# Kernel optimization log

Measured on AMD Instinct MI355X. Metric: run time of the kernel, lower is better.

The kernel has to match this reference:

```python
import jax, jax.numpy as jnp
import numpy as np

EPS = 1e-05
QN, QP = -128.0, 127.0


def setup_inputs() -> dict:
    key = jax.random.key(0)
    kx, kw = jax.random.split(key)
    x = jax.random.normal(kx, (4, 2048, 4096), dtype=jnp.float32)
    weight = jax.random.normal(kw, (4096, 4096), dtype=jnp.float32)  # [out, in]
    return {"x": x, "weight": weight}


def reference(x, weight):
    # --- per-token int8 activation quantization (activation_quant) ---
    # s: [B, S, 1], scale so that max(|x|) maps to 127
    s = QP / jnp.clip(jnp.max(jnp.abs(x), axis=-1, keepdims=True), 1e-05, None)
    q = jnp.clip(jnp.round(x * s), QN, QP)  # int8-valued, kept in float
    xq = q / s  # dequantized activations fed to the matmul

    # --- ternary weight quantization (terniarize + pack/unpack round-trip) ---
    scale_w = 1.0 / jnp.clip(jnp.mean(jnp.abs(weight)), EPS, None)
    tw = jnp.clip(jnp.round(weight * scale_w), -1.0, 1.0)  # ternary {-1,0,1}, [out, in]

    # --- bitmat: (xq) @ tw^T, then dequant by weight scale ---
    out = jnp.einsum('bsi,oi->bso', xq, tw) / scale_w
    return out
```

## Files before the change

### kernel.cpp

```cpp
#include <hip/hip_runtime.h>
#include <stdint.h>

#define K_DIM 4096
#define M_TOK 8192
#define N_OUT 4096

typedef int v4i __attribute__((ext_vector_type(4)));
typedef int v16i __attribute__((ext_vector_type(16)));


#define BAR()                                     \
    do {                                          \
        asm volatile("" ::: "memory");            \
        __builtin_amdgcn_s_barrier();             \
        asm volatile("" ::: "memory");            \
    } while (0)

__device__ __forceinline__ void gload_lds16(const void* g, void* l) {
    auto gp = reinterpret_cast<const __attribute__((address_space(1))) uint32_t*>(
        reinterpret_cast<uintptr_t>(g));
    auto lp = reinterpret_cast<__attribute__((address_space(3))) uint32_t*>(
        reinterpret_cast<uintptr_t>(l));
    __builtin_amdgcn_global_load_lds(gp, lp, 16, 0, 0);
}

__global__ __launch_bounds__(256) void quant_act(const float* __restrict__ x,
                                                 int8_t* __restrict__ q,
                                                 float* __restrict__ rs) {
    const int token = blockIdx.x;
    const int t = threadIdx.x;
    const float4* x4 = (const float4*)(x + (size_t)token * K_DIM);
    float4 v[4];
    float m = 0.0f;
#pragma unroll
    for (int r = 0; r < 4; ++r) {
        v[r] = x4[t + 256 * r];
        m = fmaxf(m, fmaxf(fmaxf(fabsf(v[r].x), fabsf(v[r].y)),
                           fmaxf(fabsf(v[r].z), fabsf(v[r].w))));
    }
#pragma unroll
    for (int off = 32; off; off >>= 1) m = fmaxf(m, __shfl_down(m, off, 64));
    __shared__ float wmax[4];
    __shared__ float smax;
    if ((t & 63) == 0) wmax[t >> 6] = m;
    __syncthreads();
    if (t == 0) smax = fmaxf(fmaxf(wmax[0], wmax[1]), fmaxf(wmax[2], wmax[3]));
    __syncthreads();
    const float s = 127.0f / fmaxf(smax, 1e-5f);
    char4* q4 = (char4*)(q + (size_t)token * K_DIM);
#pragma unroll
    for (int r = 0; r < 4; ++r) {
        float4 f = v[r];
        char4 c;
        c.x = (signed char)fminf(fmaxf(rintf(f.x * s), -128.0f), 127.0f);
        c.y = (signed char)fminf(fmaxf(rintf(f.y * s), -128.0f), 127.0f);
        c.z = (signed char)fminf(fmaxf(rintf(f.z * s), -128.0f), 127.0f);
        c.w = (signed char)fminf(fmaxf(rintf(f.w * s), -128.0f), 127.0f);
        q4[t + 256 * r] = c;
    }
    if (t == 0) rs[token] = 1.0f / s;
}

__global__ __launch_bounds__(256) void wabs_sum(const float* __restrict__ w,
                                                double* __restrict__ partial) {
    const size_t n4 = (size_t)N_OUT * K_DIM / 4;
    const size_t stride = (size_t)gridDim.x * 256;
    const float4* w4 = (const float4*)w;
    float sum = 0.0f;
    for (size_t j = (size_t)blockIdx.x * 256 + threadIdx.x; j < n4; j += stride) {
        float4 f = w4[j];
        sum += fabsf(f.x) + fabsf(f.y) + fabsf(f.z) + fabsf(f.w);
    }
    double d = (double)sum;
#pragma unroll
    for (int off = 32; off; off >>= 1) d += __shfl_down(d, off, 64);
    __shared__ double wsum[4];
    const int t = threadIdx.x;
    if ((t & 63) == 0) wsum[t >> 6] = d;
    __syncthreads();
    if (t == 0) partial[blockIdx.x] = wsum[0] + wsum[1] + wsum[2] + wsum[3];
}

__global__ __launch_bounds__(256) void ternarize(const float* __restrict__ w,
                                                 int8_t* __restrict__ tw,
                                                 const double* __restrict__ partial,
                                                 float* __restrict__ meanp) {
    const int t = threadIdx.x;
    double d = partial[t] + partial[t + 256] + partial[t + 512] + partial[t + 768];
#pragma unroll
    for (int off = 32; off; off >>= 1) d += __shfl_down(d, off, 64);
    __shared__ double pr[4];
    if ((t & 63) == 0) pr[t >> 6] = d;
    __syncthreads();
    const double tot = pr[0] + pr[1] + pr[2] + pr[3];
    const float mean = fmaxf((float)(tot * (1.0 / ((double)N_OUT * (double)K_DIM))), 1e-5f);
    const float sw = 1.0f / mean;
    if (blockIdx.x == 0 && t == 0) *meanp = mean;
    const float4* w4 = (const float4*)w;
    char4* t4 = (char4*)tw;
    const size_t base = (size_t)blockIdx.x * 1024 + t;
#pragma unroll
    for (int r = 0; r < 4; ++r) {
        float4 f = w4[base + r * 256];
        char4 c;
        c.x = (signed char)fminf(fmaxf(rintf(f.x * sw), -1.0f), 1.0f);
        c.y = (signed char)fminf(fmaxf(rintf(f.y * sw), -1.0f), 1.0f);
        c.z = (signed char)fminf(fmaxf(rintf(f.z * sw), -1.0f), 1.0f);
        c.w = (signed char)fminf(fmaxf(rintf(f.w * sw), -1.0f), 1.0f);
        t4[base + r * 256] = c;
    }
}

__global__ __launch_bounds__(512, 2) void gemm_i8(const int8_t* __restrict__ A,
                                                  const int8_t* __restrict__ B,
                                                  const float* __restrict__ rs,
                                                  const float* __restrict__ meanp,
                                                  float* __restrict__ out) {
    const int nwgx = N_OUT / 256;
    const int orig = blockIdx.y * nwgx + blockIdx.x;
    const int wg = (orig & 7) * 64 + (orig >> 3);
    const int bm = (wg / nwgx) * 256;
    const int bn = (wg % nwgx) * 256;

    __shared__ int8_t smem[4][2][16384];

    const int t0 = threadIdx.x;
    const int lane = t0 & 63;
    const int wave = t0 >> 6;
    const int wm = (wave >> 1) * 64;
    const int wn = (wave & 1) * 128;

    v16i accv[2][4] = {};

    const int R0 = t0 >> 2;
    const int scol = (((t0 & 3) ^ (R0 & 3) ^ ((R0 >> 2) & 3)) << 4);
    const int8_t* Ag = A + (size_t)(bm + R0) * K_DIM + scol;
    const int8_t* Bg = B + (size_t)(bn + R0) * K_DIM + scol;
    int8_t* ldst = &smem[0][0][0] + (size_t)t0 * 16;

    const int l31 = lane & 31;
    const int lh = lane >> 5;
    const int sx = (l31 & 3) ^ ((l31 >> 2) & 3);
    const int co0 = ((lh ^ sx) << 4);
    const int co1 = (((2 + lh) ^ sx) << 4);
    const int offA0 = (wm + l31) * 64;
    const int offA1 = (wm + 32 + l31) * 64;
    const int offB0 = (wn + l31) * 64;
    const int offB1 = (wn + 32 + l31) * 64;
    const int offB2 = (wn + 64 + l31) * 64;
    const int offB3 = (wn + 96 + l31) * 64;

#pragma unroll
    for (int pt = 0; pt < 3; ++pt) {
        const int k0 = pt * 64;
        int8_t* sb = ldst + pt * 32768;
        gload_lds16(Ag + k0, sb);
        gload_lds16(Ag + k0 + (size_t)128 * K_DIM, sb + 8192);
        gload_lds16(Bg + k0, sb + 16384);
        gload_lds16(Bg + k0 + (size_t)128 * K_DIM, sb + 24576);
    }
    asm volatile("s_waitcnt vmcnt(8)" ::: "memory");
    BAR();

    v4i ca0, ca1, cb0, cb1, cb2, cb3;
    {
        const int8_t* aB = &smem[0][0][0];
        const int8_t* bB = &smem[0][1][0];
        ca0 = *(const v4i*)(aB + offA0 + co0);
        ca1 = *(const v4i*)(aB + offA1 + co0);
        cb0 = *(const v4i*)(bB + offB0 + co0);
        cb1 = *(const v4i*)(bB + offB1 + co0);
        cb2 = *(const v4i*)(bB + offB2 + co0);
        cb3 = *(const v4i*)(bB + offB3 + co0);
    }

#pragma unroll 1
    for (int t = 0; t < 64; ++t) {
        const int slot = t & 3;
        const int8_t* aB = &smem[slot][0][0];
        const int8_t* bB = &smem[slot][1][0];

        if (t < 61) {
            const int ksg = (t + 3) * 64;
            int8_t* sb = ldst + ((t + 3) & 3) * 32768;
            gload_lds16(Ag + ksg, sb);
            gload_lds16(Ag + ksg + (size_t)128 * K_DIM, sb + 8192);
            gload_lds16(Bg + ksg, sb + 16384);
            gload_lds16(Bg + ksg + (size_t)128 * K_DIM, sb + 24576);
        }

        v4i na0 = *(const v4i*)(aB + offA0 + co1);
        v4i na1 = *(const v4i*)(aB + offA1 + co1);
        v4i nb0 = *(const v4i*)(bB + offB0 + co1);
        v4i nb1 = *(const v4i*)(bB + offB1 + co1);
        v4i nb2 = *(const v4i*)(bB + offB2 + co1);
        v4i nb3 = *(const v4i*)(bB + offB3 + co1);

        __builtin_amdgcn_s_setprio(1);
        accv[0][0] = __builtin_amdgcn_mfma_i32_32x32x32_i8(ca0, cb0, accv[0][0], 0, 0, 0);
        accv[1][0] = __builtin_amdgcn_mfma_i32_32x32x32_i8(ca1, cb0, accv[1][0], 0, 0, 0);
        accv[0][1] = __builtin_amdgcn_mfma_i32_32x32x32_i8(ca0, cb1, accv[0][1], 0, 0, 0);
        accv[1][1] = __builtin_amdgcn_mfma_i32_32x32x32_i8(ca1, cb1, accv[1][1], 0, 0, 0);
        accv[0][2] = __builtin_amdgcn_mfma_i32_32x32x32_i8(ca0, cb2, accv[0][2], 0, 0, 0);
        accv[1][2] = __builtin_amdgcn_mfma_i32_32x32x32_i8(ca1, cb2, accv[1][2], 0, 0, 0);
        accv[0][3] = __builtin_amdgcn_mfma_i32_32x32x32_i8(ca0, cb3, accv[0][3], 0, 0, 0);
        accv[1][3] = __builtin_amdgcn_mfma_i32_32x32x32_i8(ca1, cb3, accv[1][3], 0, 0, 0);
        __builtin_amdgcn_s_setprio(0);

        if (t < 61) asm volatile("s_waitcnt vmcnt(8)" ::: "memory");
        else if (t == 61) asm volatile("s_waitcnt vmcnt(4)" ::: "memory");
        else if (t == 62) asm volatile("s_waitcnt vmcnt(0)" ::: "memory");
        if (t < 63) {
            BAR();
            const int nslot = (t + 1) & 3;
            const int8_t* aN = &smem[nslot][0][0];
            const int8_t* bN = &smem[nslot][1][0];
            ca0 = *(const v4i*)(aN + offA0 + co0);
            ca1 = *(const v4i*)(aN + offA1 + co0);
            cb0 = *(const v4i*)(bN + offB0 + co0);
            cb1 = *(const v4i*)(bN + offB1 + co0);
            cb2 = *(const v4i*)(bN + offB2 + co0);
            cb3 = *(const v4i*)(bN + offB3 + co0);
        }

        __builtin_amdgcn_s_setprio(1);
        accv[0][0] = __builtin_amdgcn_mfma_i32_32x32x32_i8(na0, nb0, accv[0][0], 0, 0, 0);
        accv[1][0] = __builtin_amdgcn_mfma_i32_32x32x32_i8(na1, nb0, accv[1][0], 0, 0, 0);
        accv[0][1] = __builtin_amdgcn_mfma_i32_32x32x32_i8(na0, nb1, accv[0][1], 0, 0, 0);
        accv[1][1] = __builtin_amdgcn_mfma_i32_32x32x32_i8(na1, nb1, accv[1][1], 0, 0, 0);
        accv[0][2] = __builtin_amdgcn_mfma_i32_32x32x32_i8(na0, nb2, accv[0][2], 0, 0, 0);
        accv[1][2] = __builtin_amdgcn_mfma_i32_32x32x32_i8(na1, nb2, accv[1][2], 0, 0, 0);
        accv[0][3] = __builtin_amdgcn_mfma_i32_32x32x32_i8(na0, nb3, accv[0][3], 0, 0, 0);
        accv[1][3] = __builtin_amdgcn_mfma_i32_32x32x32_i8(na1, nb3, accv[1][3], 0, 0, 0);
        __builtin_amdgcn_s_setprio(0);
    }

    const float wmean = *meanp;
#pragma unroll
    for (int m = 0; m < 2; ++m) {
#pragma unroll
        for (int r = 0; r < 16; ++r) {
            const int row = bm + wm + m * 32 + (r & 3) + 8 * (r >> 2) + 4 * lh;
            const float scale = rs[row] * wmean;
            float* orow = out + (size_t)row * N_OUT + bn + wn + l31;
#pragma unroll
            for (int n = 0; n < 4; ++n)
                orow[n * 32] = (float)accv[m][n][r] * scale;
        }
    }
}

extern "C" void kernel_launch(void* const* d_in, const int* in_sizes, int n_in,
                              void* d_out, int out_size, void* d_ws, size_t ws_size,
                              hipStream_t stream) {
    const float* x = (const float*)d_in[0];
    const float* w = (const float*)d_in[1];
    float* out = (float*)d_out;
    char* ws = (char*)d_ws;
    int8_t* q = (int8_t*)ws;
    int8_t* tw = (int8_t*)(ws + 33554432);
    float* rs = (float*)(ws + 50331648);
    double* partial = (double*)(ws + 50364416);
    float* meanp = (float*)(ws + 50372608);

    hipLaunchKernelGGL(quant_act, dim3(M_TOK), dim3(256), 0, stream, x, q, rs);
    hipLaunchKernelGGL(wabs_sum, dim3(1024), dim3(256), 0, stream, w, partial);
    hipLaunchKernelGGL(ternarize, dim3((N_OUT * (size_t)K_DIM / 16) / 256), dim3(256), 0, stream, w, tw, partial, meanp);
    hipLaunchKernelGGL(gemm_i8, dim3(N_OUT / 256, M_TOK / 256), dim3(512), 0, stream, q, tw, rs, meanp, out);
}
```

Before: 405.1 us.

## Enlarge per-wave GEMM tile to 128x128 with four waves; one wave per token in quant

The GEMM now runs four waves per 256x256 workgroup instead of eight. Each wave computes a 128x128 sub-tile with 16 accumulators, which raises MFMA work per LDS fragment load and halves barrier participants. The cost is much higher register pressure (256 accumulator registers) and lower occupancy. The activation quant kernel now maps one wave per token and reduces with shuffle-xor only, which removes the shared memory and syncthreads step.

```diff
diff --git a/kernel.cpp b/kernel.cpp
--- a/kernel.cpp
+++ b/kernel.cpp
@@ -27,38 +27,32 @@
 __global__ __launch_bounds__(256) void quant_act(const float* __restrict__ x,
                                                  int8_t* __restrict__ q,
                                                  float* __restrict__ rs) {
-    const int token = blockIdx.x;
-    const int t = threadIdx.x;
+    const int token = blockIdx.x * 4 + (threadIdx.x >> 6);
+    const int lane = threadIdx.x & 63;
     const float4* x4 = (const float4*)(x + (size_t)token * K_DIM);
-    float4 v[4];
+    float4 v[16];
     float m = 0.0f;
 #pragma unroll
-    for (int r = 0; r < 4; ++r) {
-        v[r] = x4[t + 256 * r];
+    for (int r = 0; r < 16; ++r) {
+        v[r] = x4[lane + 64 * r];
         m = fmaxf(m, fmaxf(fmaxf(fabsf(v[r].x), fabsf(v[r].y)),
                            fmaxf(fabsf(v[r].z), fabsf(v[r].w))));
     }
 #pragma unroll
-    for (int off = 32; off; off >>= 1) m = fmaxf(m, __shfl_down(m, off, 64));
-    __shared__ float wmax[4];
-    __shared__ float smax;
-    if ((t & 63) == 0) wmax[t >> 6] = m;
-    __syncthreads();
-    if (t == 0) smax = fmaxf(fmaxf(wmax[0], wmax[1]), fmaxf(wmax[2], wmax[3]));
-    __syncthreads();
-    const float s = 127.0f / fmaxf(smax, 1e-5f);
+    for (int off = 32; off; off >>= 1) m = fmaxf(m, __shfl_xor(m, off, 64));
+    const float s = 127.0f / fmaxf(m, 1e-5f);
     char4* q4 = (char4*)(q + (size_t)token * K_DIM);
 #pragma unroll
-    for (int r = 0; r < 4; ++r) {
+    for (int r = 0; r < 16; ++r) {
         float4 f = v[r];
         char4 c;
         c.x = (signed char)fminf(fmaxf(rintf(f.x * s), -128.0f), 127.0f);
         c.y = (signed char)fminf(fmaxf(rintf(f.y * s), -128.0f), 127.0f);
         c.z = (signed char)fminf(fmaxf(rintf(f.z * s), -128.0f), 127.0f);
         c.w = (signed char)fminf(fmaxf(rintf(f.w * s), -128.0f), 127.0f);
-        q4[t + 256 * r] = c;
-    }
-    if (t == 0) rs[token] = 1.0f / s;
+        q4[lane + 64 * r] = c;
+    }
+    if (lane == 0) rs[token] = 1.0f / s;
 }
 
 __global__ __launch_bounds__(256) void wabs_sum(const float* __restrict__ w,
@@ -111,7 +105,7 @@
     }
 }
 
-__global__ __launch_bounds__(512, 2) void gemm_i8(const int8_t* __restrict__ A,
+__global__ __launch_bounds__(256, 1) void gemm_i8(const int8_t* __restrict__ A,
                                                   const int8_t* __restrict__ B,
                                                   const float* __restrict__ rs,
                                                   const float* __restrict__ meanp,
@@ -127,10 +121,10 @@
     const int t0 = threadIdx.x;
     const int lane = t0 & 63;
     const int wave = t0 >> 6;
-    const int wm = (wave >> 1) * 64;
+    const int wm = (wave >> 1) * 128;
     const int wn = (wave & 1) * 128;
 
-    v16i accv[2][4] = {};
+    v16i accv[4][4] = {};
 
     const int R0 = t0 >> 2;
     const int scol = (((t0 & 3) ^ (R0 & 3) ^ ((R0 >> 2) & 3)) << 4);
@@ -143,35 +137,37 @@
     const int sx = (l31 & 3) ^ ((l31 >> 2) & 3);
     const int co0 = ((lh ^ sx) << 4);
     const int co1 = (((2 + lh) ^ sx) << 4);
-    const int offA0 = (wm + l31) * 64;
-    const int offA1 = (wm + 32 + l31) * 64;
-    const int offB0 = (wn + l31) * 64;
-    const int offB1 = (wn + 32 + l31) * 64;
-    const int offB2 = (wn + 64 + l31) * 64;
-    const int offB3 = (wn + 96 + l31) * 64;
-
-#pragma unroll
-    for (int pt = 0; pt < 3; ++pt) {
-        const int k0 = pt * 64;
-        int8_t* sb = ldst + pt * 32768;
-        gload_lds16(Ag + k0, sb);
-        gload_lds16(Ag + k0 + (size_t)128 * K_DIM, sb + 8192);
-        gload_lds16(Bg + k0, sb + 16384);
-        gload_lds16(Bg + k0 + (size_t)128 * K_DIM, sb + 24576);
-    }
-    asm volatile("s_waitcnt vmcnt(8)" ::: "memory");
+    int offA[4], offB[4];
+#pragma unroll
+    for (int i = 0; i < 4; ++i) {
+        offA[i] = (wm + i * 32 + l31) * 64;
+        offB[i] = (wn + i * 32 + l31) * 64;
+    }
+
+#define STAGE(tile, sb)                                                       \
+    do {                                                                      \
+        const int k0_ = (tile) * 64;                                          \
+        _Pragma("unroll")                                                     \
+        for (int r_ = 0; r_ < 4; ++r_) {                                      \
+            gload_lds16(Ag + k0_ + (size_t)(64 * r_) * K_DIM, (sb) + r_ * 4096);          \
+            gload_lds16(Bg + k0_ + (size_t)(64 * r_) * K_DIM, (sb) + 16384 + r_ * 4096);  \
+        }                                                                     \
+    } while (0)
+
+#pragma unroll
+    for (int pt = 0; pt < 3; ++pt) STAGE(pt, ldst + pt * 32768);
+    asm volatile("s_waitcnt vmcnt(16)" ::: "memory");
     BAR();
 
-    v4i ca0, ca1, cb0, cb1, cb2, cb3;
+    v4i ca[4], cb[4];
     {
         const int8_t* aB = &smem[0][0][0];
         const int8_t* bB = &smem[0][1][0];
-        ca0 = *(const v4i*)(aB + offA0 + co0);
-        ca1 = *(const v4i*)(aB + offA1 + co0);
-        cb0 = *(const v4i*)(bB + offB0 + co0);
-        cb1 = *(const v4i*)(bB + offB1 + co0);
-        cb2 = *(const v4i*)(bB + offB2 + co0);
-        cb3 = *(const v4i*)(bB + offB3 + co0);
+#pragma unroll
+        for (int i = 0; i < 4; ++i) {
+            ca[i] = *(const v4i*)(aB + offA[i] + co0);
+            cb[i] = *(const v4i*)(bB + offB[i] + co0);
+        }
     }
 
 #pragma unroll 1
@@ -180,64 +176,51 @@
         const int8_t* aB = &smem[slot][0][0];
         const int8_t* bB = &smem[slot][1][0];
 
-        if (t < 61) {
-            const int ksg = (t + 3) * 64;
-            int8_t* sb = ldst + ((t + 3) & 3) * 32768;
-            gload_lds16(Ag + ksg, sb);
-            gload_lds16(Ag + ksg + (size_t)128 * K_DIM, sb + 8192);
-            gload_lds16(Bg + ksg, sb + 16384);
-            gload_lds16(Bg + ksg + (size_t)128 * K_DIM, sb + 24576);
-        }
-
-        v4i na0 = *(const v4i*)(aB + offA0 + co1);
-        v4i na1 = *(const v4i*)(aB + offA1 + co1);
-        v4i nb0 = *(const v4i*)(bB + offB0 + co1);
-        v4i nb1 = *(const v4i*)(bB + offB1 + co1);
-        v4i nb2 = *(const v4i*)(bB + offB2 + co1);
-        v4i nb3 = *(const v4i*)(bB + offB3 + co1);
+        if (t < 61) STAGE(t + 3, ldst + ((t + 3) & 3) * 32768);
+
+        v4i na[4], nb[4];
+#pragma unroll
+        for (int i = 0; i < 4; ++i) {
+            na[i] = *(const v4i*)(aB + offA[i] + co1);
+            nb[i] = *(const v4i*)(bB + offB[i] + co1);
+        }
 
         __builtin_amdgcn_s_setprio(1);
-        accv[0][0] = __builtin_amdgcn_mfma_i32_32x32x32_i8(ca0, cb0, accv[0][0], 0, 0, 0);
-        accv[1][0] = __builtin_amdgcn_mfma_i32_32x32x32_i8(ca1, cb0, accv[1][0], 0, 0, 0);
-        accv[0][1] = __builtin_amdgcn_mfma_i32_32x32x32_i8(ca0, cb1, accv[0][1], 0, 0, 0);
-        accv[1][1] = __builtin_amdgcn_mfma_i32_32x32x32_i8(ca1, cb1, accv[1][1], 0, 0, 0);
-        accv[0][2] = __builtin_amdgcn_mfma_i32_32x32x32_i8(ca0, cb2, accv[0][2], 0, 0, 0);
-        accv[1][2] = __builtin_amdgcn_mfma_i32_32x32x32_i8(ca1, cb2, accv[1][2], 0, 0, 0);
-        accv[0][3] = __builtin_amdgcn_mfma_i32_32x32x32_i8(ca0, cb3, accv[0][3], 0, 0, 0);
-        accv[1][3] = __builtin_amdgcn_mfma_i32_32x32x32_i8(ca1, cb3, accv[1][3], 0, 0, 0);
+#pragma unroll
+        for (int m = 0; m < 4; ++m)
+#pragma unroll
+            for (int n = 0; n < 4; ++n)
+                accv[m][n] = __builtin_amdgcn_mfma_i32_32x32x32_i8(ca[m], cb[n], accv[m][n], 0, 0, 0);
         __builtin_amdgcn_s_setprio(0);
 
-        if (t < 61) asm volatile("s_waitcnt vmcnt(8)" ::: "memory");
-        else if (t == 61) asm volatile("s_waitcnt vmcnt(4)" ::: "memory");
+        if (t < 61) asm volatile("s_waitcnt vmcnt(16)" ::: "memory");
+        else if (t == 61) asm volatile("s_waitcnt vmcnt(8)" ::: "memory");
         else if (t == 62) asm volatile("s_waitcnt vmcnt(0)" ::: "memory");
         if (t < 63) {
             BAR();
             const int nslot = (t + 1) & 3;
             const int8_t* aN = &smem[nslot][0][0];
             const int8_t* bN = &smem[nslot][1][0];
-            ca0 = *(const v4i*)(aN + offA0 + co0);
-            ca1 = *(const v4i*)(aN + offA1 + co0);
-            cb0 = *(const v4i*)(bN + offB0 + co0);
-            cb1 = *(const v4i*)(bN + offB1 + co0);
-            cb2 = *(const v4i*)(bN + offB2 + co0);
-            cb3 = *(const v4i*)(bN + offB3 + co0);
+#pragma unroll
+            for (int i = 0; i < 4; ++i) {
+                ca[i] = *(const v4i*)(aN + offA[i] + co0);
+                cb[i] = *(const v4i*)(bN + offB[i] + co0);
+            }
         }
 
         __builtin_amdgcn_s_setprio(1);
-        accv[0][0] = __builtin_amdgcn_mfma_i32_32x32x32_i8(na0, nb0, accv[0][0], 0, 0, 0);
-        accv[1][0] = __builtin_amdgcn_mfma_i32_32x32x32_i8(na1, nb0, accv[1][0], 0, 0, 0);
-        accv[0][1] = __builtin_amdgcn_mfma_i32_32x32x32_i8(na0, nb1, accv[0][1], 0, 0, 0);
-        accv[1][1] = __builtin_amdgcn_mfma_i32_32x32x32_i8(na1, nb1, accv[1][1], 0, 0, 0);
-        accv[0][2] = __builtin_amdgcn_mfma_i32_32x32x32_i8(na0, nb2, accv[0][2], 0, 0, 0);
-        accv[1][2] = __builtin_amdgcn_mfma_i32_32x32x32_i8(na1, nb2, accv[1][2], 0, 0, 0);
-        accv[0][3] = __builtin_amdgcn_mfma_i32_32x32x32_i8(na0, nb3, accv[0][3], 0, 0, 0);
-        accv[1][3] = __builtin_amdgcn_mfma_i32_32x32x32_i8(na1, nb3, accv[1][3], 0, 0, 0);
+#pragma unroll
+        for (int m = 0; m < 4; ++m)
+#pragma unroll
+            for (int n = 0; n < 4; ++n)
+                accv[m][n] = __builtin_amdgcn_mfma_i32_32x32x32_i8(na[m], nb[n], accv[m][n], 0, 0, 0);
         __builtin_amdgcn_s_setprio(0);
     }
+#undef STAGE
 
     const float wmean = *meanp;
 #pragma unroll
-    for (int m = 0; m < 2; ++m) {
+    for (int m = 0; m < 4; ++m) {
 #pragma unroll
         for (int r = 0; r < 16; ++r) {
             const int row = bm + wm + m * 32 + (r & 3) + 8 * (r >> 2) + 4 * lh;
@@ -263,8 +246,8 @@
     double* partial = (double*)(ws + 50364416);
     float* meanp = (float*)(ws + 50372608);
 
-    hipLaunchKernelGGL(quant_act, dim3(M_TOK), dim3(256), 0, stream, x, q, rs);
+    hipLaunchKernelGGL(quant_act, dim3(M_TOK / 4), dim3(256), 0, stream, x, q, rs);
     hipLaunchKernelGGL(wabs_sum, dim3(1024), dim3(256), 0, stream, w, partial);
     hipLaunchKernelGGL(ternarize, dim3((N_OUT * (size_t)K_DIM / 16) / 256), dim3(256), 0, stream, w, tw, partial, meanp);
-    hipLaunchKernelGGL(gemm_i8, dim3(N_OUT / 256, M_TOK / 256), dim3(512), 0, stream, q, tw, rs, meanp, out);
-}
+    hipLaunchKernelGGL(gemm_i8, dim3(N_OUT / 256, M_TOK / 256), dim3(256), 0, stream, q, tw, rs, meanp, out);
+}
```

Result: slower. 578.4 us (+42.8%).
